# Optimization experiments

Measured on AMD Instinct MI355X. Metric: run time of the kernel, lower is better.

The kernel has to match this reference:

```python
import jax, jax.numpy as jnp
import numpy as np

MODEL_DIM = 2048
NUM_EXPERTS = 64
CAPACITY_FACTOR = 1.0
NUM_TOKENS = 16384


def setup_inputs() -> dict:
    key = jax.random.key(0)
    k1, k2 = jax.random.split(key)
    inp = jax.random.normal(k1, (NUM_TOKENS, MODEL_DIM), dtype=jnp.float32)
    # wg: Linear(model_dim, num_experts, bias=False) -> weight [num_experts, model_dim]
    wg = jax.random.normal(k2, (NUM_EXPERTS, MODEL_DIM), dtype=jnp.float32) * 0.02
    return {"input": inp, "wg": wg}


def reference(input, wg):
    # logits: [N, E]
    logits = jnp.einsum('nd,ed->ne', input, wg)
    N, E = logits.shape
    # training-mode capacity: capacity_factor * ceil(N / E)
    capacity = int(CAPACITY_FACTOR * ((N + E - 1) // E))

    indices1_s = jnp.argmax(logits, axis=1)                      # [N]
    gates = jax.nn.softmax(logits, axis=1)                       # [N, E]
    mask1 = jax.nn.one_hot(indices1_s, E, dtype=gates.dtype)     # [N, E]
    gates1_s = jnp.sum(gates * mask1, axis=1)                    # [N]

    # fwd_cumsum: exclusive per-expert rank of each token (token order)
    cum = jnp.cumsum(mask1.astype(jnp.int32), axis=0)            # [N, E]
    locations1_s = (cum[jnp.arange(N), indices1_s] - 1).astype(jnp.int32)

    # float32 aux-loss branch
    me = jnp.sum(gates, axis=0)                                  # [E]
    ce = jnp.sum(mask1, axis=0)                                  # [E]
    l_aux = jnp.sum(me * ce) * (E / (N * N))

    return (l_aux, indices1_s.astype(jnp.int32), capacity, locations1_s, gates1_s, E)
```

## Files before the change

kernel.cpp:

```cpp
#include <hip/hip_runtime.h>
#include <hip/hip_bf16.h>

#define N_TOK 16384
#define DIM   2048
#define NEXP  64
#define BM    64
#define NBLK  (N_TOK / BM)
#define NKS   (DIM / 32)

#define OFF_LAUX  0
#define OFF_IDX   1
#define OFF_CAP   (1 + N_TOK)
#define OFF_LOC   (2 + N_TOK)
#define OFF_GATES (2 + 2 * N_TOK)
#define OFF_E     (2 + 3 * N_TOK)

typedef __attribute__((ext_vector_type(8))) short short8;
typedef __attribute__((ext_vector_type(4))) float f32x4;

__device__ __forceinline__ short f2bf(float x) {
    __hip_bfloat16 b = __float2bfloat16(x);
    return __builtin_bit_cast(short, b);
}
__device__ __forceinline__ float bf2f(short s) {
    __hip_bfloat16 b = __builtin_bit_cast(__hip_bfloat16, s);
    return __bfloat162float(b);
}

__global__ __launch_bounds__(256)
void prep_w_kernel(const float* __restrict__ wg,
                   short8* __restrict__ w1a,
                   short8* __restrict__ w2a,
                   short8* __restrict__ w3a)
{
    const int id = blockIdx.x * 256 + threadIdx.x;
    const int s = id >> 8;
    const int g = (id >> 6) & 3;
    const int l = id & 63;
    const int e  = 16 * g + (l & 15);
    const int k0 = 32 * s + (l >> 4) * 8;
    const float4* p = reinterpret_cast<const float4*>(wg + (size_t)e * DIM + k0);
    float4 v0 = p[0], v1 = p[1];
    float f[8] = {v0.x, v0.y, v0.z, v0.w, v1.x, v1.y, v1.z, v1.w};
    short8 b1, b2, b3;
    #pragma unroll
    for (int j = 0; j < 8; ++j) {
        b1[j] = f2bf(f[j]);
        float r = f[j] - bf2f(b1[j]);
        b2[j] = f2bf(r);
        float r2 = r - bf2f(b2[j]);
        b3[j] = f2bf(r2);
    }
    w1a[id] = b1; w2a[id] = b2; w3a[id] = b3;
}

__global__ __launch_bounds__(256)
void gate_mfma_kernel(const float* __restrict__ inp,
                      const short8* __restrict__ w1a,
                      const short8* __restrict__ w2a,
                      const short8* __restrict__ w3a,
                      float* __restrict__ out,
                      float* __restrict__ me_p,
                      int* __restrict__ hist,
                      int* __restrict__ idx_g,
                      int* __restrict__ rank_g)
{
    __shared__ float lg[BM][NEXP + 1];
    __shared__ float pme[4][NEXP];
    __shared__ int   am_s[BM];

    const int tid  = threadIdx.x;
    const int w    = tid >> 6;
    const int lane = tid & 63;
    const int blk  = blockIdx.x;
    const int row0 = blk * BM;

    const float* aptr = inp + (size_t)(row0 + 16 * w + (lane & 15)) * DIM
                        + ((lane >> 4) * 8);

    f32x4 acc[4] = {{0.f,0.f,0.f,0.f},{0.f,0.f,0.f,0.f},
                    {0.f,0.f,0.f,0.f},{0.f,0.f,0.f,0.f}};

    float4 af[4][2];
    #pragma unroll
    for (int s = 0; s < 3; ++s) {
        af[s][0] = *reinterpret_cast<const float4*>(aptr + 32 * s);
        af[s][1] = *reinterpret_cast<const float4*>(aptr + 32 * s + 4);
    }

    #pragma unroll 4
    for (int s = 0; s < NKS; ++s) {
        if (s < NKS - 3) {
            af[(s + 3) & 3][0] = *reinterpret_cast<const float4*>(aptr + 32 * (s + 3));
            af[(s + 3) & 3][1] = *reinterpret_cast<const float4*>(aptr + 32 * (s + 3) + 4);
        }
        const float4 v0 = af[s & 3][0], v1 = af[s & 3][1];
        float f[8] = {v0.x, v0.y, v0.z, v0.w, v1.x, v1.y, v1.z, v1.w};
        short8 a1, a2, a3;
        #pragma unroll
        for (int j = 0; j < 8; ++j) {
            a1[j] = f2bf(f[j]);
            float r = f[j] - bf2f(a1[j]);
            a2[j] = f2bf(r);
            float r2 = r - bf2f(a2[j]);
            a3[j] = f2bf(r2);
        }
        const int sb = s * 4 * 64 + lane;
        #pragma unroll
        for (int g = 0; g < 4; ++g) {
            short8 b1 = w1a[sb + g * 64];
            short8 b2 = w2a[sb + g * 64];
            short8 b3 = w3a[sb + g * 64];
            acc[g] = __builtin_amdgcn_mfma_f32_16x16x32_bf16(a1, b3, acc[g], 0, 0, 0);
            acc[g] = __builtin_amdgcn_mfma_f32_16x16x32_bf16(a2, b2, acc[g], 0, 0, 0);
            acc[g] = __builtin_amdgcn_mfma_f32_16x16x32_bf16(a3, b1, acc[g], 0, 0, 0);
            acc[g] = __builtin_amdgcn_mfma_f32_16x16x32_bf16(a1, b2, acc[g], 0, 0, 0);
            acc[g] = __builtin_amdgcn_mfma_f32_16x16x32_bf16(a2, b1, acc[g], 0, 0, 0);
            acc[g] = __builtin_amdgcn_mfma_f32_16x16x32_bf16(a1, b1, acc[g], 0, 0, 0);
        }
    }

    #pragma unroll
    for (int g = 0; g < 4; ++g)
        #pragma unroll
        for (int r = 0; r < 4; ++r)
            lg[16 * w + ((lane >> 4) << 2) + r][16 * g + (lane & 15)] = acc[g][r];
    __syncthreads();

    const int tok = tid >> 2;
    const int q   = tid & 3;
    float v[16];
    #pragma unroll
    for (int i = 0; i < 16; ++i) v[i] = lg[tok][q * 16 + i];
    float mx = v[0]; int ai = q * 16;
    #pragma unroll
    for (int i = 1; i < 16; ++i)
        if (v[i] > mx) { mx = v[i]; ai = q * 16 + i; }
    #pragma unroll
    for (int d = 1; d < 4; d <<= 1) {
        float om = __shfl_xor(mx, d);
        int   oi = __shfl_xor(ai, d);
        if (om > mx || (om == mx && oi < ai)) { mx = om; ai = oi; }
    }
    float p[16], sum = 0.f;
    #pragma unroll
    for (int i = 0; i < 16; ++i) { p[i] = expf(v[i] - mx); sum += p[i]; }
    #pragma unroll
    for (int d = 1; d < 4; d <<= 1) sum += __shfl_xor(sum, d);
    const float inv = 1.0f / sum;
    #pragma unroll
    for (int i = 0; i < 16; ++i) lg[tok][q * 16 + i] = p[i] * inv;
    if (q == 0) {
        am_s[tok] = ai;
        idx_g[row0 + tok] = ai;
        out[OFF_IDX + row0 + tok]   = (float)ai;
        out[OFF_GATES + row0 + tok] = inv;
    }
    __syncthreads();

    {
        const int e = tid & 63, g2 = tid >> 6;
        float a = 0.f;
        #pragma unroll
        for (int t = 0; t < 16; ++t) a += lg[g2 * 16 + t][e];
        pme[g2][e] = a;
    }
    __syncthreads();
    if (tid < NEXP)
        me_p[blk * NEXP + tid] = pme[0][tid] + pme[1][tid] + pme[2][tid] + pme[3][tid];

    if (tid < BM) {
        const int am = am_s[tid];
        const unsigned long long below = (1ull << tid) - 1ull;
        int rank = 0, cnt = 0;
        for (int e = 0; e < NEXP; ++e) {
            unsigned long long bal = __ballot(am == e);
            if (am == e)  rank = (int)__popcll(bal & below);
            if (tid == e) cnt  = (int)__popcll(bal);
        }
        rank_g[row0 + tid]    = rank;
        hist[blk * NEXP + tid] = cnt;
    }
}

__global__ __launch_bounds__(1024)
void scan_kernel(const int* __restrict__ hist,
                 int* __restrict__ offs,
                 const float* __restrict__ me_p,
                 float* __restrict__ out)
{
    __shared__ int   part[16][NEXP];
    __shared__ float pme2[16][NEXP];
    const int tid = threadIdx.x;
    const int e = tid & 63;
    const int g = tid >> 6;

    int ps = 0; float ms = 0.f;
    for (int i = 0; i < 16; ++i) {
        const int b = g * 16 + i;
        ps += hist[b * NEXP + e];
        ms += me_p[b * NEXP + e];
    }
    part[g][e] = ps;
    pme2[g][e] = ms;
    __syncthreads();

    if (tid < NEXP) {
        int run = 0; float me = 0.f;
        for (int gg = 0; gg < 16; ++gg) {
            const int v = part[gg][e];
            part[gg][e] = run;
            run += v;
            me  += pme2[gg][e];
        }
        float la = me * (float)run;
        #pragma unroll
        for (int o = 32; o > 0; o >>= 1)
            la += __shfl_down(la, o);
        if (tid == 0) {
            out[OFF_LAUX] = la * 2.384185791015625e-07f;
            out[OFF_CAP]  = 256.0f;
            out[OFF_E]    = 64.0f;
        }
    }
    __syncthreads();

    int run2 = part[g][e];
    for (int i = 0; i < 16; ++i) {
        const int b = g * 16 + i;
        offs[b * NEXP + e] = run2;
        run2 += hist[b * NEXP + e];
    }
}

__global__ __launch_bounds__(256)
void loc_kernel(const int* __restrict__ idx_g,
                const int* __restrict__ rank_g,
                const int* __restrict__ offs,
                float* __restrict__ out)
{
    int t = blockIdx.x * 256 + threadIdx.x;
    int e = idx_g[t];
    int b = t >> 6;
    out[OFF_LOC + t] = (float)(rank_g[t] + offs[b * NEXP + e]);
}

extern "C" void kernel_launch(void* const* d_in, const int* in_sizes, int n_in,
                              void* d_out, int out_size, void* d_ws, size_t ws_size,
                              hipStream_t stream)
{
    const float* inp = (const float*)d_in[0];
    const float* wg  = (const float*)d_in[1];
    float* out = (float*)d_out;

    short8* w1a = (short8*)d_ws;
    short8* w2a = w1a + 16384;
    short8* w3a = w2a + 16384;
    float* me_p = (float*)(w3a + 16384);
    int* hist   = (int*)(me_p + NBLK * NEXP);
    int* offs   = hist + NBLK * NEXP;
    int* idx_g  = offs + NBLK * NEXP;
    int* rank_g = idx_g + N_TOK;

    hipLaunchKernelGGL(prep_w_kernel, dim3(64), dim3(256), 0, stream,
                       wg, w1a, w2a, w3a);
    hipLaunchKernelGGL(gate_mfma_kernel, dim3(NBLK), dim3(256), 0, stream,
                       inp, w1a, w2a, w3a, out, me_p, hist, idx_g, rank_g);
    hipLaunchKernelGGL(scan_kernel, dim3(1), dim3(1024), 0, stream,
                       hist, offs, me_p, out);
    hipLaunchKernelGGL(loc_kernel, dim3(N_TOK / 256), dim3(256), 0, stream,
                       idx_g, rank_g, offs, out);
}
```

Measured before the change: 239.7 us.

## Split K across warps with smaller token tiles and register-prefetch gate weights

Token tiles shrink from 64 to 32 rows, doubling the block count. Within each block, two warps cover each 16-token group, each taking half of the model dimension, and the two partial logit tiles are summed in shared memory before the argmax and softmax. Gate-weight fragments are now double-buffered in registers one step ahead, and input loads run two steps ahead. The aim is more waves across the CUs and better hiding of load latency, at the cost of more registers, an extra shared-memory partial buffer, and a larger histogram and scan over twice as many blocks.

```diff
diff --git a/kernel.cpp b/kernel.cpp
--- a/kernel.cpp
+++ b/kernel.cpp
@@ -4,9 +4,11 @@
 #define N_TOK 16384
 #define DIM   2048
 #define NEXP  64
-#define BM    64
+#define BM    32
 #define NBLK  (N_TOK / BM)
-#define NKS   (DIM / 32)
+#define KSPL  2
+#define KW    (DIM / KSPL)
+#define NS    (KW / 32)
 
 #define OFF_LAUX  0
 #define OFF_IDX   1
@@ -65,36 +67,44 @@
                       int* __restrict__ idx_g,
                       int* __restrict__ rank_g)
 {
-    __shared__ float lg[BM][NEXP + 1];
+    __shared__ float lgp[KSPL][BM][NEXP + 1];
     __shared__ float pme[4][NEXP];
     __shared__ int   am_s[BM];
 
     const int tid  = threadIdx.x;
     const int w    = tid >> 6;
     const int lane = tid & 63;
+    const int tg   = w & 1;
+    const int kh   = w >> 1;
     const int blk  = blockIdx.x;
     const int row0 = blk * BM;
 
-    const float* aptr = inp + (size_t)(row0 + 16 * w + (lane & 15)) * DIM
-                        + ((lane >> 4) * 8);
+    const float* aptr = inp + (size_t)(row0 + 16 * tg + (lane & 15)) * DIM
+                        + kh * KW + ((lane >> 4) * 8);
+    const int bbase = (NS * kh) * 256 + lane;
 
     f32x4 acc[4] = {{0.f,0.f,0.f,0.f},{0.f,0.f,0.f,0.f},
                     {0.f,0.f,0.f,0.f},{0.f,0.f,0.f,0.f}};
 
-    float4 af[4][2];
-    #pragma unroll
-    for (int s = 0; s < 3; ++s) {
-        af[s][0] = *reinterpret_cast<const float4*>(aptr + 32 * s);
-        af[s][1] = *reinterpret_cast<const float4*>(aptr + 32 * s + 4);
-    }
-
-    #pragma unroll 4
-    for (int s = 0; s < NKS; ++s) {
-        if (s < NKS - 3) {
-            af[(s + 3) & 3][0] = *reinterpret_cast<const float4*>(aptr + 32 * (s + 3));
-            af[(s + 3) & 3][1] = *reinterpret_cast<const float4*>(aptr + 32 * (s + 3) + 4);
-        }
-        const float4 v0 = af[s & 3][0], v1 = af[s & 3][1];
+    float4 aA[2], aB[2];
+    short8 bA[12], bB[12];
+
+    auto loadA = [&](float4 (&buf)[2], int s) {
+        buf[0] = *reinterpret_cast<const float4*>(aptr + 32 * s);
+        buf[1] = *reinterpret_cast<const float4*>(aptr + 32 * s + 4);
+    };
+    auto loadB = [&](short8 (&buf)[12], int s) {
+        const int o = bbase + s * 256;
+        #pragma unroll
+        for (int g = 0; g < 4; ++g) {
+            buf[3 * g + 0] = w1a[o + g * 64];
+            buf[3 * g + 1] = w2a[o + g * 64];
+            buf[3 * g + 2] = w3a[o + g * 64];
+        }
+    };
+    auto step = [&](int s, float4 (&aC)[2], short8 (&bC)[12], short8 (&bO)[12]) {
+        if (s + 1 < NS) loadB(bO, s + 1);
+        const float4 v0 = aC[0], v1 = aC[1];
         float f[8] = {v0.x, v0.y, v0.z, v0.w, v1.x, v1.y, v1.z, v1.w};
         short8 a1, a2, a3;
         #pragma unroll
@@ -105,12 +115,12 @@
             float r2 = r - bf2f(a2[j]);
             a3[j] = f2bf(r2);
         }
-        const int sb = s * 4 * 64 + lane;
+        if (s + 2 < NS) loadA(aC, s + 2);
         #pragma unroll
         for (int g = 0; g < 4; ++g) {
-            short8 b1 = w1a[sb + g * 64];
-            short8 b2 = w2a[sb + g * 64];
-            short8 b3 = w3a[sb + g * 64];
+            const short8 b1 = bC[3 * g + 0];
+            const short8 b2 = bC[3 * g + 1];
+            const short8 b3 = bC[3 * g + 2];
             acc[g] = __builtin_amdgcn_mfma_f32_16x16x32_bf16(a1, b3, acc[g], 0, 0, 0);
             acc[g] = __builtin_amdgcn_mfma_f32_16x16x32_bf16(a2, b2, acc[g], 0, 0, 0);
             acc[g] = __builtin_amdgcn_mfma_f32_16x16x32_bf16(a3, b1, acc[g], 0, 0, 0);
@@ -118,38 +128,45 @@
             acc[g] = __builtin_amdgcn_mfma_f32_16x16x32_bf16(a2, b1, acc[g], 0, 0, 0);
             acc[g] = __builtin_amdgcn_mfma_f32_16x16x32_bf16(a1, b1, acc[g], 0, 0, 0);
         }
+    };
+
+    loadA(aA, 0); loadA(aB, 1); loadB(bA, 0);
+    for (int s = 0; s < NS; s += 2) {
+        step(s,     aA, bA, bB);
+        step(s + 1, aB, bB, bA);
     }
 
     #pragma unroll
     for (int g = 0; g < 4; ++g)
         #pragma unroll
         for (int r = 0; r < 4; ++r)
-            lg[16 * w + ((lane >> 4) << 2) + r][16 * g + (lane & 15)] = acc[g][r];
-    __syncthreads();
-
-    const int tok = tid >> 2;
-    const int q   = tid & 3;
-    float v[16];
-    #pragma unroll
-    for (int i = 0; i < 16; ++i) v[i] = lg[tok][q * 16 + i];
-    float mx = v[0]; int ai = q * 16;
-    #pragma unroll
-    for (int i = 1; i < 16; ++i)
-        if (v[i] > mx) { mx = v[i]; ai = q * 16 + i; }
-    #pragma unroll
-    for (int d = 1; d < 4; d <<= 1) {
+            lgp[kh][16 * tg + ((lane >> 4) << 2) + r][16 * g + (lane & 15)] = acc[g][r];
+    __syncthreads();
+
+    const int tok = tid >> 3;
+    const int q   = tid & 7;
+    float v[8];
+    #pragma unroll
+    for (int i = 0; i < 8; ++i)
+        v[i] = lgp[0][tok][8 * q + i] + lgp[1][tok][8 * q + i];
+    float mx = v[0]; int ai = 8 * q;
+    #pragma unroll
+    for (int i = 1; i < 8; ++i)
+        if (v[i] > mx) { mx = v[i]; ai = 8 * q + i; }
+    #pragma unroll
+    for (int d = 1; d < 8; d <<= 1) {
         float om = __shfl_xor(mx, d);
         int   oi = __shfl_xor(ai, d);
         if (om > mx || (om == mx && oi < ai)) { mx = om; ai = oi; }
     }
-    float p[16], sum = 0.f;
-    #pragma unroll
-    for (int i = 0; i < 16; ++i) { p[i] = expf(v[i] - mx); sum += p[i]; }
-    #pragma unroll
-    for (int d = 1; d < 4; d <<= 1) sum += __shfl_xor(sum, d);
+    float p[8], sum = 0.f;
+    #pragma unroll
+    for (int i = 0; i < 8; ++i) { p[i] = expf(v[i] - mx); sum += p[i]; }
+    #pragma unroll
+    for (int d = 1; d < 8; d <<= 1) sum += __shfl_xor(sum, d);
     const float inv = 1.0f / sum;
     #pragma unroll
-    for (int i = 0; i < 16; ++i) lg[tok][q * 16 + i] = p[i] * inv;
+    for (int i = 0; i < 8; ++i) lgp[0][tok][8 * q + i] = p[i] * inv;
     if (q == 0) {
         am_s[tok] = ai;
         idx_g[row0 + tok] = ai;
@@ -162,7 +179,7 @@
         const int e = tid & 63, g2 = tid >> 6;
         float a = 0.f;
         #pragma unroll
-        for (int t = 0; t < 16; ++t) a += lg[g2 * 16 + t][e];
+        for (int t = 0; t < 8; ++t) a += lgp[0][8 * g2 + t][e];
         pme[g2][e] = a;
     }
     __syncthreads();
@@ -172,14 +189,16 @@
     if (tid < BM) {
         const int am = am_s[tid];
         const unsigned long long below = (1ull << tid) - 1ull;
-        int rank = 0, cnt = 0;
+        int rank = 0, cl = 0, ch = 0;
         for (int e = 0; e < NEXP; ++e) {
             unsigned long long bal = __ballot(am == e);
-            if (am == e)  rank = (int)__popcll(bal & below);
-            if (tid == e) cnt  = (int)__popcll(bal);
-        }
-        rank_g[row0 + tid]    = rank;
-        hist[blk * NEXP + tid] = cnt;
+            if (am == e) rank = (int)__popcll(bal & below);
+            const int c = (int)__popcll(bal);
+            if (tid == (e & 31)) { if (e < 32) cl = c; else ch = c; }
+        }
+        rank_g[row0 + tid] = rank;
+        hist[blk * NEXP + tid]      = cl;
+        hist[blk * NEXP + tid + 32] = ch;
     }
 }
 
@@ -196,8 +215,8 @@
     const int g = tid >> 6;
 
     int ps = 0; float ms = 0.f;
-    for (int i = 0; i < 16; ++i) {
-        const int b = g * 16 + i;
+    for (int i = 0; i < 32; ++i) {
+        const int b = g * 32 + i;
         ps += hist[b * NEXP + e];
         ms += me_p[b * NEXP + e];
     }
@@ -226,8 +245,8 @@
     __syncthreads();
 
     int run2 = part[g][e];
-    for (int i = 0; i < 16; ++i) {
-        const int b = g * 16 + i;
+    for (int i = 0; i < 32; ++i) {
+        const int b = g * 32 + i;
         offs[b * NEXP + e] = run2;
         run2 += hist[b * NEXP + e];
     }
@@ -241,7 +260,7 @@
 {
     int t = blockIdx.x * 256 + threadIdx.x;
     int e = idx_g[t];
-    int b = t >> 6;
+    int b = t >> 5;
     out[OFF_LOC + t] = (float)(rank_g[t] + offs[b * NEXP + e]);
 }
 
```

New measurement: 244.3 us. Within noise of the previous version (+1.9%).
